# Kernel tuning notes

Measured on AMD Instinct MI355X. Metric: run time of the kernel, lower is better.

## Reference

```python
import jax, jax.numpy as jnp
import numpy as np

B, T, D, U = 32, 1024, 512, 512

def hard_sigmoid(x):
    # Keras hard_sigmoid: clip(0.2*x + 0.5, 0, 1)
    return jnp.clip(x * 0.2 + 0.5, 0.0, 1.0)

def setup_inputs() -> dict:
    key = jax.random.key(0)
    k1, k2, k3 = jax.random.split(key, 3)
    x = jax.random.normal(k1, (B, T, D), dtype=jnp.float32)
    kernel = jax.random.normal(k2, (D, 4 * U), dtype=jnp.float32) * 0.02
    recurrent_kernel = jax.random.normal(k3, (U, 4 * U), dtype=jnp.float32) * 0.02
    # unit_forget_bias: forget-gate slice initialized to 1
    bias = jnp.zeros((4 * U,), dtype=jnp.float32).at[U:2 * U].set(1.0)
    return {"x": x, "kernel": kernel, "recurrent_kernel": recurrent_kernel, "bias": bias}

def reference(x, kernel, recurrent_kernel, bias):
    units = recurrent_kernel.shape[0]
    batch = x.shape[0]
    # Precompute input projections for all timesteps in one big GEMM
    # (implementation=2 style): [B, T, 4U]
    xz = jnp.einsum('btd,dg->btg', x, kernel) + bias
    xz_t = jnp.transpose(xz, (1, 0, 2))  # [T, B, 4U]

    h0 = jnp.zeros((batch, units), dtype=x.dtype)
    c0 = jnp.zeros((batch, units), dtype=x.dtype)

    def step(carry, z_x):
        h, c = carry
        z = z_x + h @ recurrent_kernel  # [B, 4U]
        zi, zf, zc, zo = jnp.split(z, 4, axis=-1)
        i = hard_sigmoid(zi)
        f = hard_sigmoid(zf)
        c_new = f * c + i * jnp.tanh(zc)
        o = hard_sigmoid(zo)
        h_new = o * jnp.tanh(c_new)
        return (h_new, c_new), h_new

    (_, _), hs = jax.lax.scan(step, (h0, c0), xz_t)  # hs: [T, B, U]
    return jnp.transpose(hs, (1, 0, 2))  # [B, T, U] (return_sequences=True)
```

## Files before the change

kernel.cpp:

```cpp
#include <hip/hip_runtime.h>


#define TT 1024
#define DD 512
#define UU 512
#define NCOL 2048
#define SENT 0xFFFFFFFFu
#define RDEPTH 4

typedef float f32x2 __attribute__((ext_vector_type(2)));
typedef float f32x4 __attribute__((ext_vector_type(4)));

__device__ __forceinline__ float hsig(float v) {
  return fminf(fmaxf(0.2f * v + 0.5f, 0.0f), 1.0f);
}
__device__ __forceinline__ float tanh_fast(float x) {
  float e = __expf(2.0f * x);
  return 1.0f - 2.0f / (e + 1.0f);
}

template <bool SLEEP>
__device__ __forceinline__ void wavebar(int* ctr, int& ep) {
  asm volatile("s_waitcnt lgkmcnt(0)" ::: "memory");
  if ((threadIdx.x & 63) == 0)
    __hip_atomic_fetch_add(ctr, 1, __ATOMIC_RELAXED, __HIP_MEMORY_SCOPE_WORKGROUP);
  ep += 4;
  while (__hip_atomic_load(ctr, __ATOMIC_RELAXED, __HIP_MEMORY_SCOPE_WORKGROUP) < ep) {
    if (SLEEP) __builtin_amdgcn_s_sleep(1);
  }
  asm volatile("" ::: "memory");
}

__global__ __launch_bounds__(512, 2) void lstm_persistent(
    const float* __restrict__ x,
    const float* __restrict__ Wk,
    const float* __restrict__ Wr,
    const float* __restrict__ bias,
    float* __restrict__ out) {
  const int tid = (int)threadIdx.x;
  const int g   = (int)blockIdx.x & 7;
  const int w   = (int)blockIdx.x >> 3;
  const bool crit = (tid < 256);
  const int l   = tid & 63;

  __shared__ float LX[8][4][65];
  __shared__ float LR[2][8][4][66];
  __shared__ float RING[RDEPTH][4][66];
  __shared__ float LH[4][8][68];
  __shared__ float LB[64];
  __shared__ int cXZdone, cCRITdone, cXZbar, cCRITbar;

  if (tid == 0) { cXZdone = 0; cCRITdone = 0; cXZbar = 0; cCRITbar = 0; }
  if (tid < 64) LB[tid] = bias[(tid >> 4) * UU + w * 16 + (tid & 15)];

  f32x2 W2[64];
  {
    const int wv  = tid >> 6;
    const int idx = tid & 255;
    const int cp  = crit ? (l & 31) : (idx & 31);
    const int ko  = crit ? (2 * (wv & 3) + (l >> 5)) : (idx >> 5);
    const int gcb = (cp >> 3) * UU + w * 16 + ((2 * cp) & 15);
    const float* M = crit ? Wr : Wk;
#pragma unroll
    for (int j = 0; j < 64; ++j)
      W2[j] = *(const f32x2*)(M + (size_t)(64 * ko + j) * NCOL + gcb);
  }
  __syncthreads();

  if (crit) {
    const int wv  = tid >> 6;
    const int kq0 = 2 * wv;
    const int kql = kq0 + (l >> 5);
    const int cp  = l & 31;
    const unsigned* ou0 = (const unsigned*)out + (size_t)(g * 4 + 0) * TT * UU;
    const unsigned* ou1 = (const unsigned*)out + (size_t)(g * 4 + 1) * TT * UU;
    const unsigned* ou2 = (const unsigned*)out + (size_t)(g * 4 + 2) * TT * UU;
    const unsigned* ou3 = (const unsigned*)out + (size_t)(g * 4 + 3) * TT * UU;
    float c_state = 0.0f;
    int epC = 0;

    for (int t = 0; t < TT; ++t) {
      if (t > 0) {
        const size_t roff = (size_t)(t - 1) * UU + 128 * wv + l;
        const unsigned* p0 = ou0 + roff;
        const unsigned* p1 = ou1 + roff;
        const unsigned* p2 = ou2 + roff;
        const unsigned* p3 = ou3 + roff;
        unsigned v0, v1, v2, v3, v4, v5, v6, v7;
        for (;;) {
          asm volatile(
              "global_load_dword %0, %8, off sc0 sc1\n\t"
              "global_load_dword %1, %8, off offset:256 sc0 sc1\n\t"
              "global_load_dword %2, %9, off sc0 sc1\n\t"
              "global_load_dword %3, %9, off offset:256 sc0 sc1\n\t"
              "global_load_dword %4, %10, off sc0 sc1\n\t"
              "global_load_dword %5, %10, off offset:256 sc0 sc1\n\t"
              "global_load_dword %6, %11, off sc0 sc1\n\t"
              "global_load_dword %7, %11, off offset:256 sc0 sc1\n\t"
              "s_waitcnt vmcnt(0)"
              : "=v"(v0), "=v"(v1), "=v"(v2), "=v"(v3),
                "=v"(v4), "=v"(v5), "=v"(v6), "=v"(v7)
              : "v"(p0), "v"(p1), "v"(p2), "v"(p3)
              : "memory");
          int ok = (v0 != SENT) & (v1 != SENT) & (v2 != SENT) & (v3 != SENT) &
                   (v4 != SENT) & (v5 != SENT) & (v6 != SENT) & (v7 != SENT);
          if (__all(ok)) break;
          __builtin_amdgcn_s_sleep(16);
        }
        LH[0][kq0    ][l] = __uint_as_float(v0);
        LH[0][kq0 + 1][l] = __uint_as_float(v1);
        LH[1][kq0    ][l] = __uint_as_float(v2);
        LH[1][kq0 + 1][l] = __uint_as_float(v3);
        LH[2][kq0    ][l] = __uint_as_float(v4);
        LH[2][kq0 + 1][l] = __uint_as_float(v5);
        LH[3][kq0    ][l] = __uint_as_float(v6);
        LH[3][kq0 + 1][l] = __uint_as_float(v7);
        asm volatile("s_waitcnt lgkmcnt(0)" ::: "memory");
        __builtin_amdgcn_sched_barrier(0);
        __builtin_amdgcn_s_setprio(1);
        f32x2 a0 = {0.f, 0.f}, a1 = {0.f, 0.f}, a2 = {0.f, 0.f}, a3 = {0.f, 0.f};
#pragma unroll
        for (int j4 = 0; j4 < 16; ++j4) {
          f32x4 h0 = *(const f32x4*)&LH[0][kql][4 * j4];
          f32x4 h1 = *(const f32x4*)&LH[1][kql][4 * j4];
          f32x4 h2 = *(const f32x4*)&LH[2][kql][4 * j4];
          f32x4 h3 = *(const f32x4*)&LH[3][kql][4 * j4];
#pragma unroll
          for (int jj = 0; jj < 4; ++jj) {
            f32x2 wj = W2[4 * j4 + jj];
            a0 += (f32x2){h0[jj], h0[jj]} * wj;
            a1 += (f32x2){h1[jj], h1[jj]} * wj;
            a2 += (f32x2){h2[jj], h2[jj]} * wj;
            a3 += (f32x2){h3[jj], h3[jj]} * wj;
          }
        }
        __builtin_amdgcn_s_setprio(0);
        const int p = t & 1;
        *(f32x2*)&LR[p][kql][0][2 * cp] = a0;
        *(f32x2*)&LR[p][kql][1][2 * cp] = a1;
        *(f32x2*)&LR[p][kql][2][2 * cp] = a2;
        *(f32x2*)&LR[p][kql][3][2 * cp] = a3;
      }
      float s0 = 0.f, s1 = 0.f, s2 = 0.f, s3 = 0.f;
      if (l < 16) {
        while (__hip_atomic_load(&cXZdone, __ATOMIC_RELAXED,
                                 __HIP_MEMORY_SCOPE_WORKGROUP) < t + 1) {
        }
        asm volatile("" ::: "memory");
        const int ss = t & (RDEPTH - 1);
        s0 = RING[ss][wv][l +  0] + LB[l +  0];
        s1 = RING[ss][wv][l + 16] + LB[l + 16];
        s2 = RING[ss][wv][l + 32] + LB[l + 32];
        s3 = RING[ss][wv][l + 48] + LB[l + 48];
      }
      wavebar<false>(&cCRITbar, epC);
      if (l == 0)
        __hip_atomic_fetch_add(&cCRITdone, 1, __ATOMIC_RELAXED,
                               __HIP_MEMORY_SCOPE_WORKGROUP);
      if (l < 16) {
        if (t > 0) {
          const int p = t & 1;
#pragma unroll
          for (int kq = 0; kq < 8; ++kq) {
            s0 += LR[p][kq][wv][l +  0];
            s1 += LR[p][kq][wv][l + 16];
            s2 += LR[p][kq][wv][l + 32];
            s3 += LR[p][kq][wv][l + 48];
          }
        }
        float gi = hsig(s0);
        float gf = hsig(s1);
        float gc = tanh_fast(s2);
        float go = hsig(s3);
        c_state = gf * c_state + gi * gc;
        float h = go * tanh_fast(c_state);
        __hip_atomic_store(
            out + ((size_t)(g * 4 + wv) * TT + t) * UU + w * 16 + l, h,
            __ATOMIC_RELAXED, __HIP_MEMORY_SCOPE_AGENT);
      }
    }
  } else {
    const int idx = tid & 255;
    const int o   = idx >> 5;
    const int cp  = idx & 31;
    const float* xb0 = x + (size_t)(g * 4 + 0) * TT * DD + o * 64;
    const float* xb1 = x + (size_t)(g * 4 + 1) * TT * DD + o * 64;
    const float* xb2 = x + (size_t)(g * 4 + 2) * TT * DD + o * 64;
    const float* xb3 = x + (size_t)(g * 4 + 3) * TT * DD + o * 64;
    int epX = 0;

    for (int t = 0; t < TT; ++t) {
      const size_t off = (size_t)t * DD;
      f32x2 a0 = {0.f, 0.f}, a1 = {0.f, 0.f}, a2 = {0.f, 0.f}, a3 = {0.f, 0.f};
#pragma unroll
      for (int j4 = 0; j4 < 16; ++j4) {
        f32x4 v0 = *(const f32x4*)(xb0 + off + 4 * j4);
        f32x4 v1 = *(const f32x4*)(xb1 + off + 4 * j4);
        f32x4 v2 = *(const f32x4*)(xb2 + off + 4 * j4);
        f32x4 v3 = *(const f32x4*)(xb3 + off + 4 * j4);
#pragma unroll
        for (int jj = 0; jj < 4; ++jj) {
          f32x2 wj = W2[4 * j4 + jj];
          a0 += (f32x2){v0[jj], v0[jj]} * wj;
          a1 += (f32x2){v1[jj], v1[jj]} * wj;
          a2 += (f32x2){v2[jj], v2[jj]} * wj;
          a3 += (f32x2){v3[jj], v3[jj]} * wj;
        }
      }
      *(f32x2*)&LX[o][0][2 * cp] = a0;
      *(f32x2*)&LX[o][1][2 * cp] = a1;
      *(f32x2*)&LX[o][2][2 * cp] = a2;
      *(f32x2*)&LX[o][3][2 * cp] = a3;
      wavebar<true>(&cXZbar, epX);
      if (t >= RDEPTH) {
        while (__hip_atomic_load(&cCRITdone, __ATOMIC_RELAXED,
                                 __HIP_MEMORY_SCOPE_WORKGROUP) <
               4 * (t - RDEPTH + 1)) {
          __builtin_amdgcn_s_sleep(1);
        }
        asm volatile("" ::: "memory");
      }
      {
        const int b2 = idx >> 6, c3 = idx & 63;
        float ssum = 0.f;
#pragma unroll
        for (int oo = 0; oo < 8; ++oo) ssum += LX[oo][b2][c3];
        RING[t & (RDEPTH - 1)][b2][c3] = ssum;
      }
      wavebar<true>(&cXZbar, epX);
      if (idx == 0) {
        asm volatile("s_waitcnt lgkmcnt(0)" ::: "memory");
        __hip_atomic_fetch_add(&cXZdone, 1, __ATOMIC_RELAXED,
                               __HIP_MEMORY_SCOPE_WORKGROUP);
      }
    }
  }
}

extern "C" void kernel_launch(void* const* d_in, const int* in_sizes, int n_in,
                              void* d_out, int out_size, void* d_ws, size_t ws_size,
                              hipStream_t stream) {
  const float* x    = (const float*)d_in[0];
  const float* Wk   = (const float*)d_in[1];
  const float* Wr   = (const float*)d_in[2];
  const float* bias = (const float*)d_in[3];
  float* out = (float*)d_out;

  hipMemsetAsync(out, 0xFF, (size_t)out_size * sizeof(float), stream);
  lstm_persistent<<<256, 512, 0, stream>>>(x, Wk, Wr, bias, out);
}
```

Baseline: 4.247 ms.

## Exchange hidden state through XCD-local tagged workspace ring when group shares an XCD

At startup each block records its XCC_ID and joins a per-group counter and mask. If all 32 blocks of a batch group turn out to sit on the same XCD, hidden states are exchanged through a small 4-slot workspace ring. The ring is written and read with sc0 only, so traffic can stay in the local L2, and a per-slot tag word signals readiness, replacing sc0 sc1 sentinel polling on the output buffer. The old sentinel poll remains as a periodic fallback and as the path when blocks span XCDs. This costs an extra tag load round trip per step, extra stores, a startup rendezvous spin and two more memsets.

```diff
diff --git a/kernel.cpp b/kernel.cpp
--- a/kernel.cpp
+++ b/kernel.cpp
@@ -7,6 +7,8 @@
 #define NCOL 2048
 #define SENT 0xFFFFFFFFu
 #define RDEPTH 4
+#define SLOTS 4
+#define WS_NEED 279552
 
 typedef float f32x2 __attribute__((ext_vector_type(2)));
 typedef float f32x4 __attribute__((ext_vector_type(4)));
@@ -31,24 +33,60 @@
   asm volatile("" ::: "memory");
 }
 
+#define SENTSHOT(v0,v1,v2,v3,v4,v5,v6,v7,p0,p1,p2,p3)                    \
+  asm volatile(                                                          \
+      "global_load_dword %0, %8, off sc0 sc1\n\t"                        \
+      "global_load_dword %1, %8, off offset:256 sc0 sc1\n\t"             \
+      "global_load_dword %2, %9, off sc0 sc1\n\t"                        \
+      "global_load_dword %3, %9, off offset:256 sc0 sc1\n\t"             \
+      "global_load_dword %4, %10, off sc0 sc1\n\t"                       \
+      "global_load_dword %5, %10, off offset:256 sc0 sc1\n\t"            \
+      "global_load_dword %6, %11, off sc0 sc1\n\t"                       \
+      "global_load_dword %7, %11, off offset:256 sc0 sc1\n\t"            \
+      "s_waitcnt vmcnt(0)"                                               \
+      : "=v"(v0), "=v"(v1), "=v"(v2), "=v"(v3),                          \
+        "=v"(v4), "=v"(v5), "=v"(v6), "=v"(v7)                           \
+      : "v"(p0), "v"(p1), "v"(p2), "v"(p3)                               \
+      : "memory")
+
+#define OK8(v0,v1,v2,v3,v4,v5,v6,v7)                                     \
+  ((v0 != SENT) & (v1 != SENT) & (v2 != SENT) & (v3 != SENT) &           \
+   (v4 != SENT) & (v5 != SENT) & (v6 != SENT) & (v7 != SENT))
+
 __global__ __launch_bounds__(512, 2) void lstm_persistent(
     const float* __restrict__ x,
     const float* __restrict__ Wk,
     const float* __restrict__ Wr,
     const float* __restrict__ bias,
-    float* __restrict__ out) {
+    float* __restrict__ out,
+    int* __restrict__ wsbase) {
   const int tid = (int)threadIdx.x;
   const int g   = (int)blockIdx.x & 7;
   const int w   = (int)blockIdx.x >> 3;
   const bool crit = (tid < 256);
   const int l   = tid & 63;
+  const bool has_ws = (wsbase != nullptr);
+
+  int* tags   = wsbase;
+  int* wscnt  = wsbase + 4096;
+  int* wsmask = wsbase + 4104;
+  float* fastH = (float*)wsbase + 4352;
+
+  if (has_ws && tid == 0) {
+    unsigned xcd;
+    asm volatile("s_getreg_b32 %0, hwreg(HW_REG_XCC_ID)" : "=s"(xcd));
+    __hip_atomic_fetch_or(wsmask + g, 1u << (xcd & 31), __ATOMIC_RELAXED,
+                          __HIP_MEMORY_SCOPE_AGENT);
+    __hip_atomic_fetch_add(wscnt + g, 1, __ATOMIC_RELEASE,
+                           __HIP_MEMORY_SCOPE_AGENT);
+  }
 
   __shared__ float LX[8][4][65];
   __shared__ float LR[2][8][4][66];
   __shared__ float RING[RDEPTH][4][66];
   __shared__ float LH[4][8][68];
   __shared__ float LB[64];
-  __shared__ int cXZdone, cCRITdone, cXZbar, cCRITbar;
+  __shared__ int cXZdone, cCRITdone, cXZbar, cCRITbar, sFast;
 
   if (tid == 0) { cXZdone = 0; cCRITdone = 0; cXZbar = 0; cCRITbar = 0; }
   if (tid < 64) LB[tid] = bias[(tid >> 4) * UU + w * 16 + (tid & 15)];
@@ -65,7 +103,25 @@
     for (int j = 0; j < 64; ++j)
       W2[j] = *(const f32x2*)(M + (size_t)(64 * ko + j) * NCOL + gcb);
   }
+  if (tid == 0) {
+    int fast = 0;
+    if (has_ws) {
+      int ok = 0;
+      for (int it = 0; it < 200000; ++it) {
+        if (__hip_atomic_load(wscnt + g, __ATOMIC_ACQUIRE,
+                              __HIP_MEMORY_SCOPE_AGENT) >= 32) { ok = 1; break; }
+        __builtin_amdgcn_s_sleep(8);
+      }
+      if (ok) {
+        unsigned m = (unsigned)__hip_atomic_load(wsmask + g, __ATOMIC_RELAXED,
+                                                 __HIP_MEMORY_SCOPE_AGENT);
+        fast = (__popc(m) == 1) ? 1 : 0;
+      }
+    }
+    sFast = fast;
+  }
   __syncthreads();
+  const bool fastm = (sFast != 0);
 
   if (crit) {
     const int wv  = tid >> 6;
@@ -87,25 +143,48 @@
         const unsigned* p2 = ou2 + roff;
         const unsigned* p3 = ou3 + roff;
         unsigned v0, v1, v2, v3, v4, v5, v6, v7;
-        for (;;) {
-          asm volatile(
-              "global_load_dword %0, %8, off sc0 sc1\n\t"
-              "global_load_dword %1, %8, off offset:256 sc0 sc1\n\t"
-              "global_load_dword %2, %9, off sc0 sc1\n\t"
-              "global_load_dword %3, %9, off offset:256 sc0 sc1\n\t"
-              "global_load_dword %4, %10, off sc0 sc1\n\t"
-              "global_load_dword %5, %10, off offset:256 sc0 sc1\n\t"
-              "global_load_dword %6, %11, off sc0 sc1\n\t"
-              "global_load_dword %7, %11, off offset:256 sc0 sc1\n\t"
-              "s_waitcnt vmcnt(0)"
-              : "=v"(v0), "=v"(v1), "=v"(v2), "=v"(v3),
-                "=v"(v4), "=v"(v5), "=v"(v6), "=v"(v7)
-              : "v"(p0), "v"(p1), "v"(p2), "v"(p3)
-              : "memory");
-          int ok = (v0 != SENT) & (v1 != SENT) & (v2 != SENT) & (v3 != SENT) &
-                   (v4 != SENT) & (v5 != SENT) & (v6 != SENT) & (v7 != SENT);
-          if (__all(ok)) break;
-          __builtin_amdgcn_s_sleep(16);
+        if (fastm) {
+          const int slot = (t - 1) & (SLOTS - 1);
+          const int* tp = tags +
+              (((g * SLOTS + slot) * 32) + 8 * wv + (l & 7)) * 4 + ((l >> 3) & 3);
+          const float* fb0 = fastH + ((size_t)((g * SLOTS + slot) * 4 + 0)) * 512 + 128 * wv + l;
+          const float* fb1 = fastH + ((size_t)((g * SLOTS + slot) * 4 + 1)) * 512 + 128 * wv + l;
+          const float* fb2 = fastH + ((size_t)((g * SLOTS + slot) * 4 + 2)) * 512 + 128 * wv + l;
+          const float* fb3 = fastH + ((size_t)((g * SLOTS + slot) * 4 + 3)) * 512 + 128 * wv + l;
+          int miss = 0;
+          for (;;) {
+            int tg;
+            asm volatile("global_load_dword %0, %1, off sc0\n\ts_waitcnt vmcnt(0)"
+                         : "=v"(tg) : "v"(tp) : "memory");
+            if (__all(tg == t - 1)) {
+              asm volatile(
+                  "global_load_dword %0, %8, off sc0\n\t"
+                  "global_load_dword %1, %8, off offset:256 sc0\n\t"
+                  "global_load_dword %2, %9, off sc0\n\t"
+                  "global_load_dword %3, %9, off offset:256 sc0\n\t"
+                  "global_load_dword %4, %10, off sc0\n\t"
+                  "global_load_dword %5, %10, off offset:256 sc0\n\t"
+                  "global_load_dword %6, %11, off sc0\n\t"
+                  "global_load_dword %7, %11, off offset:256 sc0\n\t"
+                  "s_waitcnt vmcnt(0)"
+                  : "=v"(v0), "=v"(v1), "=v"(v2), "=v"(v3),
+                    "=v"(v4), "=v"(v5), "=v"(v6), "=v"(v7)
+                  : "v"(fb0), "v"(fb1), "v"(fb2), "v"(fb3)
+                  : "memory");
+              break;
+            }
+            if (((++miss) & 7) == 0) {
+              SENTSHOT(v0, v1, v2, v3, v4, v5, v6, v7, p0, p1, p2, p3);
+              if (__all(OK8(v0, v1, v2, v3, v4, v5, v6, v7))) break;
+            }
+            __builtin_amdgcn_s_sleep(1);
+          }
+        } else {
+          for (;;) {
+            SENTSHOT(v0, v1, v2, v3, v4, v5, v6, v7, p0, p1, p2, p3);
+            if (__all(OK8(v0, v1, v2, v3, v4, v5, v6, v7))) break;
+            __builtin_amdgcn_s_sleep(16);
+          }
         }
         LH[0][kq0    ][l] = __uint_as_float(v0);
         LH[0][kq0 + 1][l] = __uint_as_float(v1);
@@ -174,6 +253,19 @@
         float go = hsig(s3);
         c_state = gf * c_state + gi * gc;
         float h = go * tanh_fast(c_state);
+        if (fastm) {
+          float* fp = fastH +
+              ((size_t)((g * SLOTS + (t & (SLOTS - 1))) * 4 + wv)) * 512 + 16 * w + l;
+          asm volatile("global_store_dword %0, %1, off sc0"
+                       :: "v"(fp), "v"(h) : "memory");
+          asm volatile("s_waitcnt vmcnt(0)" ::: "memory");
+          if (l == 0) {
+            int tv = t;
+            int* tq = tags + (((g * SLOTS + (t & (SLOTS - 1))) * 32) + w) * 4 + wv;
+            asm volatile("global_store_dword %0, %1, off sc0"
+                         :: "v"(tq), "v"(tv) : "memory");
+          }
+        }
         __hip_atomic_store(
             out + ((size_t)(g * 4 + wv) * TT + t) * UU + w * 16 + l, h,
             __ATOMIC_RELAXED, __HIP_MEMORY_SCOPE_AGENT);
@@ -246,6 +338,12 @@
   const float* bias = (const float*)d_in[3];
   float* out = (float*)d_out;
 
+  int* wsbase = nullptr;
+  if (ws_size >= (size_t)WS_NEED) {
+    wsbase = (int*)d_ws;
+    hipMemsetAsync(wsbase, 0xFF, 16384, stream);
+    hipMemsetAsync((char*)d_ws + 16384, 0x00, 64, stream);
+  }
   hipMemsetAsync(out, 0xFF, (size_t)out_size * sizeof(float), stream);
-  lstm_persistent<<<256, 512, 0, stream>>>(x, Wk, Wr, bias, out);
-}
+  lstm_persistent<<<256, 512, 0, stream>>>(x, Wk, Wr, bias, out, wsbase);
+}
```

Measured after the change: 4.561 ms. +7.4%, slower.
